# Performance work log

Hardware: AMD Instinct MI355X
Metric: run time of the kernel (lower is better)

Reference implementation:

```python
import jax, jax.numpy as jnp
import numpy as np

BITS = 4
GROUPSIZE = 128
IN_FEATURES = 4096
OUT_FEATURES = 11008
PACK = 32 // BITS  # 8 nibbles per int32
MASK = (1 << BITS) - 1


def setup_inputs() -> dict:
    key = jax.random.key(0)
    k_x, k_qw, k_qz, k_s, k_b = jax.random.split(key, 5)
    n_groups = IN_FEATURES // GROUPSIZE  # 32
    x = jax.random.normal(k_x, (2, 2048, IN_FEATURES), dtype=jnp.float32)
    # packed int32 buffers: random bit patterns (each int32 holds 8 4-bit values)
    qweight = jax.random.randint(k_qw, (IN_FEATURES // 32 * BITS, OUT_FEATURES),
                                 -2**31, 2**31 - 1, dtype=jnp.int32)
    qzeros = jax.random.randint(k_qz, (n_groups, OUT_FEATURES // 32 * BITS),
                                -2**31, 2**31 - 1, dtype=jnp.int32)
    scales = jax.random.uniform(k_s, (n_groups, OUT_FEATURES), dtype=jnp.float32,
                                minval=0.001, maxval=0.02)
    bias = jax.random.normal(k_b, (OUT_FEATURES,), dtype=jnp.float32) * 0.01
    return {"x": x, "qweight": qweight, "scales": scales, "qzeros": qzeros, "bias": bias}


def _dequant(qweight, scales, qzeros):
    # shift amounts for each packed nibble: [0,4,...,28]
    wf = jnp.arange(0, 32, BITS, dtype=jnp.int32)
    n_groups = scales.shape[0]
    # unpack zeros: [G, out//8] -> [G, out//8, 8] -> [G, 1, out]
    zeros = jnp.bitwise_and(jnp.right_shift(qzeros[:, :, None], wf[None, None, :]), MASK)
    zeros = zeros.reshape(n_groups, 1, OUT_FEATURES).astype(scales.dtype)
    # unpack weights: [in//8, out] -> [in//8, 8, out] -> [G, groupsize, out]
    w = jnp.bitwise_and(jnp.right_shift(qweight[:, None, :], wf[None, :, None]), MASK)
    w = w.reshape(n_groups, GROUPSIZE, OUT_FEATURES).astype(scales.dtype)
    sc = scales[:, None, :]  # [G, 1, out]
    weight = sc * w - sc * zeros  # scales*w - scale_zeros
    return weight.reshape(IN_FEATURES, OUT_FEATURES)


def reference(x, qweight, scales, qzeros, bias):
    weight = _dequant(qweight, scales, qzeros)
    return jnp.matmul(x, weight) + bias
```

## Files before the change

kernel.cpp:

```cpp
#include <hip/hip_runtime.h>
#include <cstdint>
#include <cstddef>

#define IN_F 4096
#define OUT_F 11008
#define M_ROWS 4096
#define QZ_STRIDE (OUT_F / 8)
#define NKT (IN_F / 128)
#define NGROUPS 32

typedef __attribute__((ext_vector_type(4))) float f32x4;
typedef __attribute__((ext_vector_type(4))) int i32x4;
typedef __attribute__((ext_vector_type(8))) __bf16 bf16x8;
typedef uint32_t u32;
typedef uint16_t u16;
typedef uint8_t u8;

__device__ __forceinline__ u16 f2bf(float f) {
  u32 u = __builtin_bit_cast(u32, f);
  u += 0x7FFFu + ((u >> 16) & 1u);
  return (u16)(u >> 16);
}

__global__ __launch_bounds__(256) void conv_x_i8(const float* __restrict__ x,
                                                 u8* __restrict__ xq,
                                                 float* __restrict__ xs) {
  const int row = blockIdx.x;
  const int tid = threadIdx.x;
  const float* xr = x + (size_t)row * IN_F;
  float4 v[4];
#pragma unroll
  for (int j = 0; j < 4; ++j)
    v[j] = reinterpret_cast<const float4*>(xr)[tid * 4 + j];
  float am = 0.f;
#pragma unroll
  for (int j = 0; j < 4; ++j)
    am = fmaxf(am, fmaxf(fmaxf(fabsf(v[j].x), fabsf(v[j].y)),
                         fmaxf(fabsf(v[j].z), fabsf(v[j].w))));
#pragma unroll
  for (int off = 32; off > 0; off >>= 1) am = fmaxf(am, __shfl_xor(am, off, 64));
  __shared__ float wmax[4];
  if ((tid & 63) == 0) wmax[tid >> 6] = am;
  __syncthreads();
  am = fmaxf(fmaxf(wmax[0], wmax[1]), fmaxf(wmax[2], wmax[3]));
  const float amc = fmaxf(am, 1e-30f);
  const float inv = 127.f / amc;
  if (tid == 0) xs[row] = amc / 127.f;
  u32 o[4];
#pragma unroll
  for (int j = 0; j < 4; ++j) {
    u32 b0 = (u32)(u8)(int8_t)__float2int_rn(v[j].x * inv);
    u32 b1 = (u32)(u8)(int8_t)__float2int_rn(v[j].y * inv);
    u32 b2 = (u32)(u8)(int8_t)__float2int_rn(v[j].z * inv);
    u32 b3 = (u32)(u8)(int8_t)__float2int_rn(v[j].w * inv);
    o[j] = b0 | (b1 << 8) | (b2 << 16) | (b3 << 24);
  }
  *reinterpret_cast<uint4*>(xq + (size_t)row * IN_F + tid * 16) =
      make_uint4(o[0], o[1], o[2], o[3]);
}

__global__ void colscale_kernel(const float* __restrict__ scl,
                                float* __restrict__ Scol,
                                float* __restrict__ invScol) {
  const int n = blockIdx.x * 256 + threadIdx.x;
  if (n >= OUT_F) return;
  float m = 0.f;
#pragma unroll 4
  for (int g = 0; g < NGROUPS; ++g) m = fmaxf(m, scl[(size_t)g * OUT_F + n]);
  const float S = m * (15.f / 127.f);
  Scol[n] = S;
  invScol[n] = 1.f / S;
}

__global__ void dequant_i8(const int* __restrict__ qw, const int* __restrict__ qz,
                           const float* __restrict__ scl,
                           const float* __restrict__ invScol,
                           u8* __restrict__ wq8) {
  const int nl = threadIdx.x & 31, rl = threadIdx.x >> 5;
  const int n = blockIdx.x * 32 + nl;
  const int r = blockIdx.y * 8 + rl;
  const int g = r >> 4;
  u32 q = (u32)qw[(size_t)r * OUT_F + n];
  const int z = (int)(((u32)qz[g * QZ_STRIDE + (n >> 3)] >> (4 * (n & 7))) & 15u);
  const float si = scl[(size_t)g * OUT_F + n] * invScol[n];
  u32 lo = 0, hi = 0;
#pragma unroll
  for (int e = 0; e < 4; ++e) {
    float f = fminf(fmaxf((float)((int)((q >> (4 * e)) & 15u) - z) * si, -127.f), 127.f);
    lo |= ((u32)(u8)(int8_t)__float2int_rn(f)) << (8 * e);
  }
#pragma unroll
  for (int e = 0; e < 4; ++e) {
    float f = fminf(fmaxf((float)((int)((q >> (16 + 4 * e)) & 15u) - z) * si, -127.f), 127.f);
    hi |= ((u32)(u8)(int8_t)__float2int_rn(f)) << (8 * e);
  }
  *reinterpret_cast<uint2*>(wq8 + (size_t)n * IN_F + r * 8) = make_uint2(lo, hi);
}

__global__ __launch_bounds__(512, 2) void gemm256_i8(
    const u8* __restrict__ xq, const u8* __restrict__ wq,
    const float* __restrict__ Scol, const float* __restrict__ xs,
    const float* __restrict__ bias, float* __restrict__ out) {
  __shared__ __align__(16) u8 As[2][256 * 128];
  __shared__ __align__(16) u8 Bs[2][256 * 128];
  const int tid = threadIdx.x;
  const int lane = tid & 63, wid = tid >> 6;
  const int cpx = (int)gridDim.x >> 3;
  const int swz = ((int)blockIdx.x & 7) * cpx + ((int)blockIdx.x >> 3);
  const int m0 = (swz & 15) * 256, n0 = (swz >> 4) * 256;
  const int wr = wid >> 2, wc = wid & 3;
  const int frow = lane & 15, q4 = lane >> 4, f7 = lane & 7;
  const int lrow = lane >> 3, ls = lane & 7;

  const int colb0 = ((q4 ^ f7) << 4);
  const int colb1 = (((4 | q4) ^ f7) << 4);
  const int arowB = (wr * 128 + frow) * 128;
  const int browB = (wc * 64 + frow) * 128;

  const u8* gA = xq + (size_t)(m0 + lrow) * IN_F + ((ls ^ lrow) << 4);
  const u8* gB = wq + (size_t)(n0 + lrow) * IN_F + ((ls ^ lrow) << 4);
  const int rsbase = (wid >> 2) * 128 + (wid & 3) * 16;

  i32x4 acc[8][4] = {};
  i32x4 af[4][2], bf[4][2];

  auto stage = [&](u8* ldsb, const u8* gl, int u, int h) {
#pragma unroll
    for (int j = 0; j < 2; ++j) {
      const int rowstart = rsbase + j * 8 + h * 64;
      __builtin_amdgcn_global_load_lds(
          (__attribute__((address_space(1))) void*)(gl + (size_t)rowstart * IN_F + (size_t)u * 128),
          (__attribute__((address_space(3))) void*)(ldsb + rowstart * 128), 16, 0, 0);
    }
  };

  stage(Bs[0], gB, 0, 0);
  stage(Bs[0], gB, 0, 1);
  stage(As[0], gA, 0, 0);
  stage(As[0], gA, 0, 1);
  stage(Bs[1], gB, 1, 0);
  stage(Bs[1], gB, 1, 1);
  stage(As[1], gA, 1, 0);
  stage(As[1], gA, 1, 1);
  asm volatile("s_waitcnt vmcnt(8)" ::: "memory");
  __builtin_amdgcn_s_barrier();
  {
    const u8* Ac = As[0];
    const u8* Bc = Bs[0];
#pragma unroll
    for (int mi = 0; mi < 4; ++mi) {
      af[mi][0] = *reinterpret_cast<const i32x4*>(Ac + arowB + mi * 2048 + colb0);
      af[mi][1] = *reinterpret_cast<const i32x4*>(Ac + arowB + mi * 2048 + colb1);
    }
#pragma unroll
    for (int ni = 0; ni < 2; ++ni) {
      bf[ni][0] = *reinterpret_cast<const i32x4*>(Bc + browB + ni * 2048 + colb0);
      bf[ni][1] = *reinterpret_cast<const i32x4*>(Bc + browB + ni * 2048 + colb1);
    }
  }
  asm volatile("s_waitcnt lgkmcnt(0)" ::: "memory");

  for (int u = 0; u < NKT; ++u) {
    const int cur = u & 1;
    const u8* Ac = As[cur];
    const u8* Bc = Bs[cur];
    const u8* An = As[cur ^ 1];
    const u8* Bn = Bs[cur ^ 1];
    const bool stT = (u + 2 < NKT);

    __builtin_amdgcn_s_barrier();
    __builtin_amdgcn_s_setprio(1);
#pragma unroll
    for (int mi = 0; mi < 4; ++mi)
#pragma unroll
      for (int ni = 0; ni < 2; ++ni) {
        acc[mi][ni] = __builtin_amdgcn_mfma_i32_16x16x64_i8(af[mi][0], bf[ni][0], acc[mi][ni], 0, 0, 0);
        acc[mi][ni] = __builtin_amdgcn_mfma_i32_16x16x64_i8(af[mi][1], bf[ni][1], acc[mi][ni], 0, 0, 0);
      }
    __builtin_amdgcn_s_setprio(0);
#pragma unroll
    for (int ni = 0; ni < 2; ++ni) {
      bf[2 + ni][0] = *reinterpret_cast<const i32x4*>(Bc + browB + (2 + ni) * 2048 + colb0);
      bf[2 + ni][1] = *reinterpret_cast<const i32x4*>(Bc + browB + (2 + ni) * 2048 + colb1);
    }
    asm volatile("s_waitcnt lgkmcnt(0)" ::: "memory");

    __builtin_amdgcn_s_barrier();
    __builtin_amdgcn_s_setprio(1);
#pragma unroll
    for (int mi = 0; mi < 4; ++mi)
#pragma unroll
      for (int ni = 0; ni < 2; ++ni) {
        acc[mi][2 + ni] = __builtin_amdgcn_mfma_i32_16x16x64_i8(af[mi][0], bf[2 + ni][0], acc[mi][2 + ni], 0, 0, 0);
        acc[mi][2 + ni] = __builtin_amdgcn_mfma_i32_16x16x64_i8(af[mi][1], bf[2 + ni][1], acc[mi][2 + ni], 0, 0, 0);
      }
    __builtin_amdgcn_s_setprio(0);
#pragma unroll
    for (int mi = 0; mi < 4; ++mi) {
      af[mi][0] = *reinterpret_cast<const i32x4*>(Ac + arowB + (4 + mi) * 2048 + colb0);
      af[mi][1] = *reinterpret_cast<const i32x4*>(Ac + arowB + (4 + mi) * 2048 + colb1);
    }
    if (stT) stage(Bs[cur], gB, u + 2, 0);
    asm volatile("s_waitcnt lgkmcnt(0)" ::: "memory");

    __builtin_amdgcn_s_barrier();
    __builtin_amdgcn_s_setprio(1);
#pragma unroll
    for (int mi = 0; mi < 4; ++mi)
#pragma unroll
      for (int ni = 0; ni < 2; ++ni) {
        acc[4 + mi][ni] = __builtin_amdgcn_mfma_i32_16x16x64_i8(af[mi][0], bf[ni][0], acc[4 + mi][ni], 0, 0, 0);
        acc[4 + mi][ni] = __builtin_amdgcn_mfma_i32_16x16x64_i8(af[mi][1], bf[ni][1], acc[4 + mi][ni], 0, 0, 0);
      }
    __builtin_amdgcn_s_setprio(0);
    if (stT) {
      stage(Bs[cur], gB, u + 2, 1);
      stage(As[cur], gA, u + 2, 0);
      stage(As[cur], gA, u + 2, 1);
    }
    if (stT)
      asm volatile("s_waitcnt vmcnt(8)" ::: "memory");
    else
      asm volatile("s_waitcnt vmcnt(0)" ::: "memory");

    __builtin_amdgcn_s_barrier();
    __builtin_amdgcn_s_setprio(1);
#pragma unroll
    for (int mi = 0; mi < 4; ++mi)
#pragma unroll
      for (int ni = 0; ni < 2; ++ni) {
        acc[4 + mi][2 + ni] = __builtin_amdgcn_mfma_i32_16x16x64_i8(af[mi][0], bf[2 + ni][0], acc[4 + mi][2 + ni], 0, 0, 0);
        acc[4 + mi][2 + ni] = __builtin_amdgcn_mfma_i32_16x16x64_i8(af[mi][1], bf[2 + ni][1], acc[4 + mi][2 + ni], 0, 0, 0);
      }
    __builtin_amdgcn_s_setprio(0);
    if (u + 1 < NKT) {
#pragma unroll
      for (int mi = 0; mi < 4; ++mi) {
        af[mi][0] = *reinterpret_cast<const i32x4*>(An + arowB + mi * 2048 + colb0);
        af[mi][1] = *reinterpret_cast<const i32x4*>(An + arowB + mi * 2048 + colb1);
      }
#pragma unroll
      for (int ni = 0; ni < 2; ++ni) {
        bf[ni][0] = *reinterpret_cast<const i32x4*>(Bn + browB + ni * 2048 + colb0);
        bf[ni][1] = *reinterpret_cast<const i32x4*>(Bn + browB + ni * 2048 + colb1);
      }
      asm volatile("s_waitcnt lgkmcnt(0)" ::: "memory");
    }
  }

  const int crow = (lane >> 4) * 4, ccol = lane & 15;
#pragma unroll
  for (int mi = 0; mi < 8; ++mi) {
    const int rowb = m0 + wr * 128 + mi * 16 + crow;
    float sxv[4];
#pragma unroll
    for (int r2 = 0; r2 < 4; ++r2) sxv[r2] = xs[rowb + r2];
#pragma unroll
    for (int ni = 0; ni < 4; ++ni) {
      const int col = n0 + wc * 64 + ni * 16 + ccol;
      const float bv = bias[col];
      const float sv = Scol[col];
#pragma unroll
      for (int r2 = 0; r2 < 4; ++r2)
        __builtin_nontemporal_store(
            fmaf(sxv[r2] * sv, (float)acc[mi][ni][r2], bv),
            out + (size_t)(rowb + r2) * OUT_F + col);
    }
  }
}

__global__ __launch_bounds__(256, 2) void gemm_fused(
    const float* __restrict__ x, const int* __restrict__ qw,
    const int* __restrict__ qz, const float* __restrict__ sc,
    const float* __restrict__ bias, float* __restrict__ out) {
  __shared__ u16 Asb[128 * 64];
  __shared__ u16 Bsb[128 * 64];
  const int tid = threadIdx.x;
  const int lane = tid & 63, wid = tid >> 6;
  const int bm = blockIdx.x & 31, bn = blockIdx.x >> 5;
  const int m0 = bm * 128, n0 = bn * 128;
  const int wr = wid >> 1, wc = wid & 1;
  const int frow = lane & 15, fk = (lane >> 4) * 8;
  f32x4 acc[4][4] = {};

  for (int kt = 0; kt < 64; ++kt) {
    const int k0 = kt * 64;
#pragma unroll
    for (int it = 0; it < 8; ++it) {
      int c = it * 256 + tid;
      int row = c >> 4, c4 = c & 15;
      float4 v = *reinterpret_cast<const float4*>(
          x + (size_t)(m0 + row) * IN_F + k0 + c4 * 4);
      uint2 o;
      o.x = (u32)f2bf(v.x) | ((u32)f2bf(v.y) << 16);
      o.y = (u32)f2bf(v.z) | ((u32)f2bf(v.w) << 16);
      *reinterpret_cast<uint2*>(Asb + row * 64 + c4 * 4) = o;
    }
    {
      int nl = tid & 127, rq = tid >> 7;
      int n = n0 + nl;
      int gq = k0 >> 7;
      int z = (int)(((u32)qz[gq * QZ_STRIDE + (n >> 3)] >> (4 * (n & 7))) & 15u);
      float s = sc[gq * OUT_F + n];
#pragma unroll
      for (int j = 0; j < 4; ++j) {
        int r = (k0 >> 3) + rq * 4 + j;
        u32 q = (u32)qw[(size_t)r * OUT_F + n];
        u32 o[4];
#pragma unroll
        for (int e = 0; e < 4; ++e) {
          u16 lo = f2bf(s * (float)((int)((q >> (8 * e)) & 15u) - z));
          u16 hi = f2bf(s * (float)((int)((q >> (8 * e + 4)) & 15u) - z));
          o[e] = (u32)lo | ((u32)hi << 16);
        }
        *reinterpret_cast<uint4*>(Bsb + nl * 64 + (rq * 4 + j) * 8) =
            make_uint4(o[0], o[1], o[2], o[3]);
      }
    }
    __syncthreads();
#pragma unroll
    for (int kk = 0; kk < 64; kk += 32) {
      bf16x8 a[4], b[4];
#pragma unroll
      for (int mi = 0; mi < 4; ++mi)
        a[mi] = *reinterpret_cast<const bf16x8*>(Asb + (wr * 64 + mi * 16 + frow) * 64 + kk + fk);
#pragma unroll
      for (int ni = 0; ni < 4; ++ni)
        b[ni] = *reinterpret_cast<const bf16x8*>(Bsb + (wc * 64 + ni * 16 + frow) * 64 + kk + fk);
#pragma unroll
      for (int mi = 0; mi < 4; ++mi)
#pragma unroll
        for (int ni = 0; ni < 4; ++ni)
          acc[mi][ni] = __builtin_amdgcn_mfma_f32_16x16x32_bf16(a[mi], b[ni], acc[mi][ni], 0, 0, 0);
    }
    __syncthreads();
  }
  const int crow = (lane >> 4) * 4, ccol = lane & 15;
#pragma unroll
  for (int mi = 0; mi < 4; ++mi) {
#pragma unroll
    for (int ni = 0; ni < 4; ++ni) {
      int col = n0 + wc * 64 + ni * 16 + ccol;
      float bv = bias[col];
      int rowb = m0 + wr * 64 + mi * 16 + crow;
#pragma unroll
      for (int r2 = 0; r2 < 4; ++r2)
        out[(size_t)(rowb + r2) * OUT_F + col] = acc[mi][ni][r2] + bv;
    }
  }
}

extern "C" void kernel_launch(void* const* d_in, const int* in_sizes, int n_in,
                              void* d_out, int out_size, void* d_ws, size_t ws_size,
                              hipStream_t stream) {
  const float* x = (const float*)d_in[0];
  const int* qw = (const int*)d_in[1];
  const float* sc = (const float*)d_in[2];
  const int* qz = (const int*)d_in[3];
  const float* bias = (const float*)d_in[4];
  float* out = (float*)d_out;

  const size_t xq_bytes = (size_t)M_ROWS * IN_F;
  const size_t wq_bytes = (size_t)OUT_F * IN_F;
  const size_t xs_bytes = (size_t)M_ROWS * 4;
  const size_t sc_bytes = (size_t)OUT_F * 4;

  if (ws_size >= xq_bytes + wq_bytes + xs_bytes + 2 * sc_bytes) {
    u8* xqp = (u8*)d_ws;
    u8* wqp = (u8*)d_ws + xq_bytes;
    float* xsp = (float*)((u8*)d_ws + xq_bytes + wq_bytes);
    float* Scolp = (float*)((u8*)d_ws + xq_bytes + wq_bytes + xs_bytes);
    float* invScolp = Scolp + OUT_F;
    hipLaunchKernelGGL(conv_x_i8, dim3(M_ROWS), dim3(256), 0, stream, x, xqp, xsp);
    hipLaunchKernelGGL(colscale_kernel, dim3((OUT_F + 255) / 256), dim3(256), 0,
                       stream, sc, Scolp, invScolp);
    hipLaunchKernelGGL(dequant_i8, dim3(OUT_F / 32, 512 / 8), dim3(256), 0,
                       stream, qw, qz, sc, invScolp, wqp);
    hipLaunchKernelGGL(gemm256_i8, dim3((M_ROWS / 256) * (OUT_F / 256)),
                       dim3(512), 0, stream, xqp, wqp, Scolp, xsp, bias, out);
  } else {
    hipLaunchKernelGGL(gemm_fused, dim3(32 * 86), dim3(256), 0, stream, x, qw,
                       qz, sc, bias, out);
  }
}
```

Baseline: 249.5 us.

## Restructure int8 GEMM main loop into two phases with full B fragments

```diff
diff --git a/kernel.cpp b/kernel.cpp
--- a/kernel.cpp
+++ b/kernel.cpp
@@ -122,7 +122,7 @@
   const int rsbase = (wid >> 2) * 128 + (wid & 3) * 16;
 
   i32x4 acc[8][4] = {};
-  i32x4 af[4][2], bf[4][2];
+  i32x4 af[4][2], ah[4][2], bf[4][2];
 
   auto stage = [&](u8* ldsb, const u8* gl, int u, int h) {
 #pragma unroll
@@ -148,73 +148,59 @@
     const u8* Ac = As[0];
     const u8* Bc = Bs[0];
 #pragma unroll
+    for (int ni = 0; ni < 4; ++ni) {
+      bf[ni][0] = *reinterpret_cast<const i32x4*>(Bc + browB + ni * 2048 + colb0);
+      bf[ni][1] = *reinterpret_cast<const i32x4*>(Bc + browB + ni * 2048 + colb1);
+    }
+#pragma unroll
     for (int mi = 0; mi < 4; ++mi) {
       af[mi][0] = *reinterpret_cast<const i32x4*>(Ac + arowB + mi * 2048 + colb0);
       af[mi][1] = *reinterpret_cast<const i32x4*>(Ac + arowB + mi * 2048 + colb1);
     }
-#pragma unroll
-    for (int ni = 0; ni < 2; ++ni) {
-      bf[ni][0] = *reinterpret_cast<const i32x4*>(Bc + browB + ni * 2048 + colb0);
-      bf[ni][1] = *reinterpret_cast<const i32x4*>(Bc + browB + ni * 2048 + colb1);
-    }
-  }
-  asm volatile("s_waitcnt lgkmcnt(0)" ::: "memory");
+  }
 
   for (int u = 0; u < NKT; ++u) {
     const int cur = u & 1;
     const u8* Ac = As[cur];
-    const u8* Bc = Bs[cur];
     const u8* An = As[cur ^ 1];
     const u8* Bn = Bs[cur ^ 1];
     const bool stT = (u + 2 < NKT);
 
     __builtin_amdgcn_s_barrier();
+    asm volatile("s_waitcnt lgkmcnt(0)" ::: "memory");
+    __builtin_amdgcn_sched_barrier(0);
     __builtin_amdgcn_s_setprio(1);
 #pragma unroll
     for (int mi = 0; mi < 4; ++mi)
 #pragma unroll
-      for (int ni = 0; ni < 2; ++ni) {
+      for (int ni = 0; ni < 4; ++ni) {
         acc[mi][ni] = __builtin_amdgcn_mfma_i32_16x16x64_i8(af[mi][0], bf[ni][0], acc[mi][ni], 0, 0, 0);
         acc[mi][ni] = __builtin_amdgcn_mfma_i32_16x16x64_i8(af[mi][1], bf[ni][1], acc[mi][ni], 0, 0, 0);
       }
     __builtin_amdgcn_s_setprio(0);
-#pragma unroll
-    for (int ni = 0; ni < 2; ++ni) {
-      bf[2 + ni][0] = *reinterpret_cast<const i32x4*>(Bc + browB + (2 + ni) * 2048 + colb0);
-      bf[2 + ni][1] = *reinterpret_cast<const i32x4*>(Bc + browB + (2 + ni) * 2048 + colb1);
-    }
+    if (stT) {
+      stage(Bs[cur], gB, u + 2, 0);
+      stage(Bs[cur], gB, u + 2, 1);
+    }
+#pragma unroll
+    for (int mi = 0; mi < 4; ++mi) {
+      ah[mi][0] = *reinterpret_cast<const i32x4*>(Ac + arowB + (4 + mi) * 2048 + colb0);
+      ah[mi][1] = *reinterpret_cast<const i32x4*>(Ac + arowB + (4 + mi) * 2048 + colb1);
+    }
+
+    __builtin_amdgcn_s_barrier();
     asm volatile("s_waitcnt lgkmcnt(0)" ::: "memory");
-
-    __builtin_amdgcn_s_barrier();
+    __builtin_amdgcn_sched_barrier(0);
     __builtin_amdgcn_s_setprio(1);
 #pragma unroll
     for (int mi = 0; mi < 4; ++mi)
 #pragma unroll
-      for (int ni = 0; ni < 2; ++ni) {
-        acc[mi][2 + ni] = __builtin_amdgcn_mfma_i32_16x16x64_i8(af[mi][0], bf[2 + ni][0], acc[mi][2 + ni], 0, 0, 0);
-        acc[mi][2 + ni] = __builtin_amdgcn_mfma_i32_16x16x64_i8(af[mi][1], bf[2 + ni][1], acc[mi][2 + ni], 0, 0, 0);
-      }
-    __builtin_amdgcn_s_setprio(0);
-#pragma unroll
-    for (int mi = 0; mi < 4; ++mi) {
-      af[mi][0] = *reinterpret_cast<const i32x4*>(Ac + arowB + (4 + mi) * 2048 + colb0);
-      af[mi][1] = *reinterpret_cast<const i32x4*>(Ac + arowB + (4 + mi) * 2048 + colb1);
-    }
-    if (stT) stage(Bs[cur], gB, u + 2, 0);
-    asm volatile("s_waitcnt lgkmcnt(0)" ::: "memory");
-
-    __builtin_amdgcn_s_barrier();
-    __builtin_amdgcn_s_setprio(1);
-#pragma unroll
-    for (int mi = 0; mi < 4; ++mi)
-#pragma unroll
-      for (int ni = 0; ni < 2; ++ni) {
-        acc[4 + mi][ni] = __builtin_amdgcn_mfma_i32_16x16x64_i8(af[mi][0], bf[ni][0], acc[4 + mi][ni], 0, 0, 0);
-        acc[4 + mi][ni] = __builtin_amdgcn_mfma_i32_16x16x64_i8(af[mi][1], bf[ni][1], acc[4 + mi][ni], 0, 0, 0);
+      for (int ni = 0; ni < 4; ++ni) {
+        acc[4 + mi][ni] = __builtin_amdgcn_mfma_i32_16x16x64_i8(ah[mi][0], bf[ni][0], acc[4 + mi][ni], 0, 0, 0);
+        acc[4 + mi][ni] = __builtin_amdgcn_mfma_i32_16x16x64_i8(ah[mi][1], bf[ni][1], acc[4 + mi][ni], 0, 0, 0);
       }
     __builtin_amdgcn_s_setprio(0);
     if (stT) {
-      stage(Bs[cur], gB, u + 2, 1);
       stage(As[cur], gA, u + 2, 0);
       stage(As[cur], gA, u + 2, 1);
     }
@@ -222,29 +208,17 @@
       asm volatile("s_waitcnt vmcnt(8)" ::: "memory");
     else
       asm volatile("s_waitcnt vmcnt(0)" ::: "memory");
-
-    __builtin_amdgcn_s_barrier();
-    __builtin_amdgcn_s_setprio(1);
-#pragma unroll
-    for (int mi = 0; mi < 4; ++mi)
-#pragma unroll
-      for (int ni = 0; ni < 2; ++ni) {
-        acc[4 + mi][2 + ni] = __builtin_amdgcn_mfma_i32_16x16x64_i8(af[mi][0], bf[2 + ni][0], acc[4 + mi][2 + ni], 0, 0, 0);
-        acc[4 + mi][2 + ni] = __builtin_amdgcn_mfma_i32_16x16x64_i8(af[mi][1], bf[2 + ni][1], acc[4 + mi][2 + ni], 0, 0, 0);
-      }
-    __builtin_amdgcn_s_setprio(0);
     if (u + 1 < NKT) {
+#pragma unroll
+      for (int ni = 0; ni < 4; ++ni) {
+        bf[ni][0] = *reinterpret_cast<const i32x4*>(Bn + browB + ni * 2048 + colb0);
+        bf[ni][1] = *reinterpret_cast<const i32x4*>(Bn + browB + ni * 2048 + colb1);
+      }
 #pragma unroll
       for (int mi = 0; mi < 4; ++mi) {
         af[mi][0] = *reinterpret_cast<const i32x4*>(An + arowB + mi * 2048 + colb0);
         af[mi][1] = *reinterpret_cast<const i32x4*>(An + arowB + mi * 2048 + colb1);
       }
-#pragma unroll
-      for (int ni = 0; ni < 2; ++ni) {
-        bf[ni][0] = *reinterpret_cast<const i32x4*>(Bn + browB + ni * 2048 + colb0);
-        bf[ni][1] = *reinterpret_cast<const i32x4*>(Bn + browB + ni * 2048 + colb1);
-      }
-      asm volatile("s_waitcnt lgkmcnt(0)" ::: "memory");
     }
   }
 
```

New measurement: 248.8 us. About the same (-0.3%).
